# Kernel optimization log

Hardware: AMD Instinct MI355X
Metric: run time of the kernel (lower is better)

## Reference

```python
import jax, jax.numpy as jnp
import numpy as np
from jax import lax

K = 3
PAD = 1
DIL = 1
BN_EPS = 1e-5


def setup_inputs() -> dict:
    key = jax.random.key(0)
    ks = jax.random.split(key, 7)
    B, C, O, H, W = 4, 64, 64, 128, 128
    x = jax.random.normal(ks[0], (B, C, H, W), jnp.float32)
    # offset conv params (zero-init in the module; small random here to exercise bilinear sampling)
    w_off = jax.random.normal(ks[1], (2 * K * K, C, K, K), jnp.float32) * 0.01
    b_off = jax.random.normal(ks[2], (2 * K * K,), jnp.float32) * 0.01
    # deformable conv params
    w_dcn = jax.random.normal(ks[3], (O, C, K, K), jnp.float32) / np.sqrt(C * K * K).astype(np.float32)
    b_dcn = jax.random.normal(ks[4], (O,), jnp.float32) * 0.01
    # BatchNorm affine params
    gamma = 1.0 + 0.1 * jax.random.normal(ks[5], (O,), jnp.float32)
    beta = 0.1 * jax.random.normal(ks[6], (O,), jnp.float32)
    return dict(x=x, w_off=w_off, b_off=b_off, w_dcn=w_dcn, b_dcn=b_dcn, gamma=gamma, beta=beta)


def _conv2d(x, w):
    return lax.conv_general_dilated(
        x, w, window_strides=(1, 1), padding=[(PAD, PAD), (PAD, PAD)],
        rhs_dilation=(DIL, DIL), dimension_numbers=('NCHW', 'OIHW', 'NCHW'))


def _gather(x, iy, ix):
    # x: [B,C,H,W]; iy/ix: [B,K2,H,W] int32 (already clipped in-range)
    B, C, H, W = x.shape
    idx = (iy * W + ix).reshape(B, -1)          # [B, K2*H*W]
    xf = x.reshape(B, C, H * W)
    v = jax.vmap(lambda xb, ib: xb[:, ib])(xf, idx)  # [B, C, K2*H*W]
    return v.reshape(B, C, iy.shape[1], H, W)


def _deform_sample(x, offset):
    # torchvision DeformConv2d v1: offsets are (dy, dx) pairs per kernel tap, zero-padding bilinear.
    B, C, H, W = x.shape
    K2 = K * K
    off = offset.reshape(B, K2, 2, H, W)
    ky = jnp.repeat(jnp.arange(K), K)   # tap row index, k = ky*K + kx
    kx = jnp.tile(jnp.arange(K), K)
    py = off[:, :, 0] + (ky * DIL - PAD)[None, :, None, None] + jnp.arange(H)[None, None, :, None]
    px = off[:, :, 1] + (kx * DIL - PAD)[None, :, None, None] + jnp.arange(W)[None, None, None, :]
    y0 = jnp.floor(py)
    x0 = jnp.floor(px)
    wy = py - y0
    wx = px - x0
    y0i = y0.astype(jnp.int32)
    x0i = x0.astype(jnp.int32)
    acc = jnp.zeros((B, C, K2, H, W), x.dtype)
    for dy, dx in ((0, 0), (0, 1), (1, 0), (1, 1)):
        iy = y0i + dy
        ix = x0i + dx
        wgt = (wy if dy else 1.0 - wy) * (wx if dx else 1.0 - wx)
        valid = (iy >= 0) & (iy < H) & (ix >= 0) & (ix < W)
        v = _gather(x, jnp.clip(iy, 0, H - 1), jnp.clip(ix, 0, W - 1))
        acc = acc + v * (wgt * valid.astype(x.dtype))[:, None]
    return acc  # [B, C, K2, H, W]


def reference(x, w_off, b_off, w_dcn, b_dcn, gamma, beta):
    offset = _conv2d(x, w_off) + b_off[None, :, None, None]
    patches = _deform_sample(x, offset)                     # [B,C,K2,H,W]
    O = w_dcn.shape[0]
    out = jnp.einsum('bckhw,ock->bohw', patches, w_dcn.reshape(O, -1, K * K))
    out = out + b_dcn[None, :, None, None]
    # BatchNorm2d in training mode: biased batch statistics over (B,H,W)
    mean = out.mean(axis=(0, 2, 3), keepdims=True)
    var = out.var(axis=(0, 2, 3), keepdims=True)
    out = (out - mean) * lax.rsqrt(var + BN_EPS)
    out = out * gamma[None, :, None, None] + beta[None, :, None, None]
    return jax.nn.relu(out)
```

## Files before the change

kernel.cpp:

```cpp
#include <hip/hip_runtime.h>

#define HW   16384
#define WID  128
#define HEI  128
#define CIN  64
#define OCH  64

typedef __attribute__((ext_vector_type(8))) short bf16x8;
typedef __attribute__((ext_vector_type(4))) float f32x4;
typedef __attribute__((ext_vector_type(4))) int   i32x4;

__device__ __forceinline__ unsigned short f2bf(float f) {
    unsigned u = __float_as_uint(f);
    u += 0x7FFF + ((u >> 16) & 1);
    return (unsigned short)(u >> 16);
}
__device__ __forceinline__ float bf2f(short s) {
    return __uint_as_float(((unsigned)(unsigned short)s) << 16);
}

__global__ __launch_bounds__(256) void kprep(const float* __restrict__ x,
                                             const float* __restrict__ wdcn,
                                             const float* __restrict__ woff,
                                             unsigned short* __restrict__ xt,
                                             unsigned short* __restrict__ wpack,
                                             unsigned short* __restrict__ woffpack) {
    int blk = blockIdx.x;
    if (blk < 256) {
        int gp = blk * 256 + threadIdx.x;
        int b = gp >> 14;
        int hw = gp & (HW - 1);
        const float* xb = x + (size_t)b * CIN * HW + hw;
        unsigned short* o = xt + ((size_t)gp << 6);
#pragma unroll
        for (int c8 = 0; c8 < 8; c8++) {
            bf16x8 v;
#pragma unroll
            for (int j = 0; j < 8; j++)
                v[j] = (short)f2bf(xb[(size_t)(c8 * 8 + j) * HW]);
            *(bf16x8*)(o + c8 * 8) = v;
        }
    } else {
        int t = (blk - 256) * 256 + threadIdx.x;
        if (t < 36864) {
            int j  = t & 7;
            int l  = (t >> 3) & 63;
            int nt = (t >> 9) & 3;
            int s  = t >> 11;
            int k  = s * 32 + (l >> 4) * 8 + j;
            int o  = nt * 16 + (l & 15);
            int tap = k >> 6, c = k & 63;
            wpack[t] = f2bf(wdcn[o * 576 + c * 9 + tap]);
        } else {
            int u  = t - 36864;
            int j  = u & 7;
            int l  = (u >> 3) & 63;
            int nt = (u >> 9) & 1;
            int s  = u >> 10;
            int k  = s * 32 + (l >> 4) * 8 + j;
            int o  = nt * 16 + (l & 15);
            int tap = k >> 6, c = k & 63;
            float v = (o < 18) ? woff[o * 576 + c * 9 + tap] : 0.f;
            woffpack[u] = f2bf(v);
        }
    }
}

__global__ __launch_bounds__(256, 3) void kdcn(const unsigned short* __restrict__ xt,
                                               const unsigned short* __restrict__ wpack,
                                               const unsigned short* __restrict__ woffpack,
                                               const float* __restrict__ boff,
                                               const float* __restrict__ bdcn,
                                               float* __restrict__ conv,
                                               float* __restrict__ part) {
    __shared__ __align__(16) unsigned char smem[48384];

    int tid = threadIdx.x;
    int lane = tid & 63, wave = tid >> 6;
    int lr = lane & 15, hi = lane >> 4;

    int pixg = blockIdx.x * 32;
    int b = pixg >> 14;
    int hwb = pixg & (HW - 1);
    int h = hwb >> 7;
    int w0 = hwb & (WID - 1);

    {
        int g = lane >> 3, sub = lane & 7;
        int px = wave * 8 + g;
        int w = w0 + px;
        const unsigned char* xtb =
            (const unsigned char*)xt + (((size_t)b * HW) << 7) + sub * 16;
        unsigned char* prow = smem + px * 1152;
        unsigned swz = (unsigned)((px & 7) << 4);
#pragma unroll
        for (int tap = 0; tap < 9; tap++) {
            int sy = h + tap / 3 - 1;
            int sx = w + tap % 3 - 1;
            bool ok = ((unsigned)sy < HEI) && ((unsigned)sx < WID);
            bf16x8 v = {0, 0, 0, 0, 0, 0, 0, 0};
            if (ok) v = *(const bf16x8*)(xtb + ((sy * WID + sx) << 7));
            *(bf16x8*)(prow + ((unsigned)(tap * 128 + sub * 16) ^ swz)) = v;
        }
    }
    __syncthreads();

    {
        int mw = wave & 1, nw = wave >> 1;
        int oc = nw * 16 + lr;
        float ob = (oc < 18) ? boff[oc] : 0.f;
        f32x4 oacc = {ob, ob, ob, ob};
        unsigned swzr = (unsigned)((lr & 7) << 4);
        const unsigned short* wop = woffpack + (size_t)(nw * 64 + lane) * 8;
        int arow = (mw * 16 + lr) * 1152;
#pragma unroll
        for (int s = 0; s < 18; s++) {
            unsigned inblk = (unsigned)((s >> 1) * 128)
                           + (((unsigned)((s & 1) * 64 + hi * 16)) ^ swzr);
            bf16x8 a  = *(const bf16x8*)(smem + arow + inblk);
            bf16x8 wf = *(const bf16x8*)(wop + (size_t)s * 1024);
            oacc = __builtin_amdgcn_mfma_f32_16x16x32_bf16(a, wf, oacc, 0, 0, 0);
        }
        float* offLds = (float*)(smem + 46080);
        if (oc < 18) {
#pragma unroll
            for (int r = 0; r < 4; r++)
                offLds[(mw * 16 + hi * 4 + r) * 18 + oc] = oacc[r];
        }
    }
    __syncthreads();

    int* ti = (int*)(smem + 36864);
    {
        const float* offLds = (const float*)(smem + 46080);
        for (int item = tid; item < 288; item += 256) {
            int ppx = item / 9, tap = item - ppx * 9;
            float dy = offLds[ppx * 18 + tap * 2];
            float dx = offLds[ppx * 18 + tap * 2 + 1];
            float py  = dy + (float)(h + tap / 3 - 1);
            float pxf = dx + (float)(w0 + ppx + tap % 3 - 1);
            float y0f = floorf(py), x0f = floorf(pxf);
            float wy = py - y0f, wx = pxf - x0f;
            int y0 = (int)y0f, x0 = (int)x0f;
            float wy0 = ((unsigned)y0       < HEI) ? 1.f - wy : 0.f;
            float wy1 = ((unsigned)(y0 + 1) < HEI) ? wy       : 0.f;
            float wx0 = ((unsigned)x0       < WID) ? 1.f - wx : 0.f;
            float wx1 = ((unsigned)(x0 + 1) < WID) ? wx       : 0.f;
            int yc0 = min(max(y0, 0),     HEI - 1) * WID;
            int yc1 = min(max(y0 + 1, 0), HEI - 1) * WID;
            int xc0 = min(max(x0, 0),     WID - 1);
            int xc1 = min(max(x0 + 1, 0), WID - 1);
            int* t8 = ti + item * 8;
            t8[0] = (yc0 + xc0) << 7;
            t8[1] = (yc0 + xc1) << 7;
            t8[2] = (yc1 + xc0) << 7;
            t8[3] = (yc1 + xc1) << 7;
            float* f8 = (float*)t8;
            f8[4] = wy0 * wx0; f8[5] = wy0 * wx1;
            f8[6] = wy1 * wx0; f8[7] = wy1 * wx1;
        }
    }
    __syncthreads();

    bf16x8 bfrag[18];
    const unsigned short* wp = wpack + (size_t)(wave * 64 + lane) * 8;
#pragma unroll
    for (int s = 0; s < 18; s++)
        bfrag[s] = *(const bf16x8*)(wp + (size_t)s * 2048);
    float bias = bdcn[wave * 16 + lr];

    {
        int g = lane >> 3, sub = lane & 7;
        int px = wave * 8 + g;
        const unsigned char* xtb =
            (const unsigned char*)xt + (((size_t)b * HW) << 7) + sub * 16;
        unsigned char* prow = smem + px * 1152;
        unsigned swz = (unsigned)((px & 7) << 4);
        const int* tbase = ti + px * 72;
#pragma unroll
        for (int tap = 0; tap < 9; tap++) {
            i32x4 t4 = *(const i32x4*)(tbase + tap * 8);
            f32x4 w4 = *(const f32x4*)(tbase + tap * 8 + 4);
            bf16x8 c00 = *(const bf16x8*)(xtb + t4[0]);
            bf16x8 c01 = *(const bf16x8*)(xtb + t4[1]);
            bf16x8 c10 = *(const bf16x8*)(xtb + t4[2]);
            bf16x8 c11 = *(const bf16x8*)(xtb + t4[3]);
            bf16x8 v;
#pragma unroll
            for (int j = 0; j < 8; j++) {
                float sv = w4[0] * bf2f(c00[j]) + w4[1] * bf2f(c01[j])
                         + w4[2] * bf2f(c10[j]) + w4[3] * bf2f(c11[j]);
                v[j] = (short)f2bf(sv);
            }
            *(bf16x8*)(prow + ((unsigned)(tap * 128 + sub * 16) ^ swz)) = v;
        }
    }
    __syncthreads();

    f32x4 acc0 = {bias, bias, bias, bias};
    f32x4 acc1 = acc0;
    unsigned swzr = (unsigned)((lr & 7) << 4);
#pragma unroll
    for (int s = 0; s < 18; s++) {
        unsigned inblk = (unsigned)((s >> 1) * 128)
                       + (((unsigned)((s & 1) * 64 + hi * 16)) ^ swzr);
        bf16x8 a0 = *(const bf16x8*)(smem + lr * 1152 + inblk);
        bf16x8 a1 = *(const bf16x8*)(smem + (16 + lr) * 1152 + inblk);
        acc0 = __builtin_amdgcn_mfma_f32_16x16x32_bf16(a0, bfrag[s], acc0, 0, 0, 0);
        acc1 = __builtin_amdgcn_mfma_f32_16x16x32_bf16(a1, bfrag[s], acc1, 0, 0, 0);
    }
    __syncthreads();

    float* ldsC = (float*)smem;
    {
        int o = wave * 16 + lr;
        int pxb = hi * 4;
#pragma unroll
        for (int r = 0; r < 4; r++) {
            ldsC[o * 33 + pxb + r]      = acc0[r];
            ldsC[o * 33 + 16 + pxb + r] = acc1[r];
        }
    }
    __syncthreads();
    {
        int px4 = (tid & 7) * 4;
#pragma unroll
        for (int pass = 0; pass < 2; pass++) {
            int oo = (tid >> 3) + pass * 32;
            float4 v;
            v.x = ldsC[oo * 33 + px4];
            v.y = ldsC[oo * 33 + px4 + 1];
            v.z = ldsC[oo * 33 + px4 + 2];
            v.w = ldsC[oo * 33 + px4 + 3];
            *(float4*)(conv + ((size_t)b * OCH + oo) * HW + hwb + px4) = v;
        }
    }

    {
        float s  = acc0[0] + acc0[1] + acc0[2] + acc0[3]
                 + acc1[0] + acc1[1] + acc1[2] + acc1[3];
        float s2 = acc0[0]*acc0[0] + acc0[1]*acc0[1] + acc0[2]*acc0[2] + acc0[3]*acc0[3]
                 + acc1[0]*acc1[0] + acc1[1]*acc1[1] + acc1[2]*acc1[2] + acc1[3]*acc1[3];
        s  += __shfl_xor(s, 16);  s2 += __shfl_xor(s2, 16);
        s  += __shfl_xor(s, 32);  s2 += __shfl_xor(s2, 32);
        if (hi == 0) {
            int c = wave * 16 + lr;
            part[(size_t)c * 2048 + blockIdx.x]        = s;
            part[(size_t)(64 + c) * 2048 + blockIdx.x] = s2;
        }
    }
}

__global__ __launch_bounds__(256) void kred(const float* __restrict__ part,
                                            float* __restrict__ stats) {
    int row = blockIdx.x;
    int tid = threadIdx.x;
    const float* p = part + (size_t)row * 2048;
    float s = 0.f;
#pragma unroll
    for (int i = 0; i < 8; i++) s += p[tid + i * 256];
#pragma unroll
    for (int d = 1; d < 64; d <<= 1) s += __shfl_xor(s, d);
    __shared__ float red[4];
    if ((tid & 63) == 0) red[tid >> 6] = s;
    __syncthreads();
    if (tid == 0) stats[row] = red[0] + red[1] + red[2] + red[3];
}

__global__ __launch_bounds__(256) void kapply(float* __restrict__ conv,
                                              const float* __restrict__ stats,
                                              const float* __restrict__ gamma,
                                              const float* __restrict__ beta) {
    int t = blockIdx.x * 256 + threadIdx.x;
    int c = (t >> 12) & 63;
    float mean = stats[c] * (1.f / 65536.f);
    float var  = stats[64 + c] * (1.f / 65536.f) - mean * mean;
    float rstd = rsqrtf(var + 1e-5f);
    float sc = rstd * gamma[c];
    float sh = beta[c] - mean * sc;
    float4 v = ((float4*)conv)[t];
    float4 r;
    r.x = fmaxf(v.x * sc + sh, 0.f);
    r.y = fmaxf(v.y * sc + sh, 0.f);
    r.z = fmaxf(v.z * sc + sh, 0.f);
    r.w = fmaxf(v.w * sc + sh, 0.f);
    ((float4*)conv)[t] = r;
}

extern "C" void kernel_launch(void* const* d_in, const int* in_sizes, int n_in,
                              void* d_out, int out_size, void* d_ws, size_t ws_size,
                              hipStream_t stream) {
    const float* x     = (const float*)d_in[0];
    const float* woff  = (const float*)d_in[1];
    const float* boff  = (const float*)d_in[2];
    const float* wdcn  = (const float*)d_in[3];
    const float* bdcn  = (const float*)d_in[4];
    const float* gamma = (const float*)d_in[5];
    const float* beta  = (const float*)d_in[6];
    float* out = (float*)d_out;

    unsigned char* ws = (unsigned char*)d_ws;
    unsigned short* xt       = (unsigned short*)ws;
    unsigned short* wpack    = (unsigned short*)(ws + 8388608);
    unsigned short* woffpack = (unsigned short*)(ws + 8462336);
    float*          part     = (float*)(ws + 8499200);
    float*          stats    = (float*)(ws + 9547776);

    hipLaunchKernelGGL(kprep,  dim3(472),  dim3(256), 0, stream,
                       x, wdcn, woff, xt, wpack, woffpack);
    hipLaunchKernelGGL(kdcn,   dim3(2048), dim3(256), 0, stream,
                       xt, wpack, woffpack, boff, bdcn, out, part);
    hipLaunchKernelGGL(kred,   dim3(128),  dim3(256), 0, stream, part, stats);
    hipLaunchKernelGGL(kapply, dim3(4096), dim3(256), 0, stream,
                       out, stats, gamma, beta);
}
```

Baseline: 56.52 us.

## Compute bilinear sampling coefficients per lane and drop LDS tap table

Removes the shared-memory table of per-tap gather indices and bilinear weights. Each of the 8 lanes that handle one pixel now recomputes the coordinates and weights from the offset LDS values. This drops one barrier and shrinks LDS from about 48 KB to 39 KB, so the launch bound is raised to 4 blocks per CU. It also hoists the weight-fragment loads ahead of the barrier. The cost is redundant ALU work per lane and higher register pressure, which could cause spills under the tighter occupancy bound.

After: 56.88 us. Within noise of the previous version (+0.6%).

```diff
diff --git a/kernel.cpp b/kernel.cpp
--- a/kernel.cpp
+++ b/kernel.cpp
@@ -66,14 +66,14 @@
     }
 }
 
-__global__ __launch_bounds__(256, 3) void kdcn(const unsigned short* __restrict__ xt,
+__global__ __launch_bounds__(256, 4) void kdcn(const unsigned short* __restrict__ xt,
                                                const unsigned short* __restrict__ wpack,
                                                const unsigned short* __restrict__ woffpack,
                                                const float* __restrict__ boff,
                                                const float* __restrict__ bdcn,
                                                float* __restrict__ conv,
                                                float* __restrict__ part) {
-    __shared__ __align__(16) unsigned char smem[48384];
+    __shared__ __align__(16) unsigned char smem[39168];
 
     int tid = threadIdx.x;
     int lane = tid & 63, wave = tid >> 6;
@@ -121,24 +121,37 @@
             bf16x8 wf = *(const bf16x8*)(wop + (size_t)s * 1024);
             oacc = __builtin_amdgcn_mfma_f32_16x16x32_bf16(a, wf, oacc, 0, 0, 0);
         }
-        float* offLds = (float*)(smem + 46080);
+        float* offLds = (float*)(smem + 36864);
         if (oc < 18) {
 #pragma unroll
             for (int r = 0; r < 4; r++)
                 offLds[(mw * 16 + hi * 4 + r) * 18 + oc] = oacc[r];
         }
     }
-    __syncthreads();
-
-    int* ti = (int*)(smem + 36864);
-    {
-        const float* offLds = (const float*)(smem + 46080);
-        for (int item = tid; item < 288; item += 256) {
-            int ppx = item / 9, tap = item - ppx * 9;
-            float dy = offLds[ppx * 18 + tap * 2];
-            float dx = offLds[ppx * 18 + tap * 2 + 1];
+
+    bf16x8 bfrag[18];
+    const unsigned short* wp = wpack + (size_t)(wave * 64 + lane) * 8;
+#pragma unroll
+    for (int s = 0; s < 18; s++)
+        bfrag[s] = *(const bf16x8*)(wp + (size_t)s * 2048);
+    float bias = bdcn[wave * 16 + lr];
+    __syncthreads();
+
+    {
+        int g = lane >> 3, sub = lane & 7;
+        int px = wave * 8 + g;
+        int w = w0 + px;
+        const unsigned char* xtb =
+            (const unsigned char*)xt + (((size_t)b * HW) << 7) + sub * 16;
+        unsigned char* prow = smem + px * 1152;
+        unsigned swz = (unsigned)((px & 7) << 4);
+        const float* offL = (const float*)(smem + 36864) + px * 18;
+#pragma unroll
+        for (int tap = 0; tap < 9; tap++) {
+            float dy = offL[tap * 2];
+            float dx = offL[tap * 2 + 1];
             float py  = dy + (float)(h + tap / 3 - 1);
-            float pxf = dx + (float)(w0 + ppx + tap % 3 - 1);
+            float pxf = dx + (float)(w + tap % 3 - 1);
             float y0f = floorf(py), x0f = floorf(pxf);
             float wy = py - y0f, wx = pxf - x0f;
             int y0 = (int)y0f, x0 = (int)x0f;
@@ -150,46 +163,17 @@
             int yc1 = min(max(y0 + 1, 0), HEI - 1) * WID;
             int xc0 = min(max(x0, 0),     WID - 1);
             int xc1 = min(max(x0 + 1, 0), WID - 1);
-            int* t8 = ti + item * 8;
-            t8[0] = (yc0 + xc0) << 7;
-            t8[1] = (yc0 + xc1) << 7;
-            t8[2] = (yc1 + xc0) << 7;
-            t8[3] = (yc1 + xc1) << 7;
-            float* f8 = (float*)t8;
-            f8[4] = wy0 * wx0; f8[5] = wy0 * wx1;
-            f8[6] = wy1 * wx0; f8[7] = wy1 * wx1;
-        }
-    }
-    __syncthreads();
-
-    bf16x8 bfrag[18];
-    const unsigned short* wp = wpack + (size_t)(wave * 64 + lane) * 8;
-#pragma unroll
-    for (int s = 0; s < 18; s++)
-        bfrag[s] = *(const bf16x8*)(wp + (size_t)s * 2048);
-    float bias = bdcn[wave * 16 + lr];
-
-    {
-        int g = lane >> 3, sub = lane & 7;
-        int px = wave * 8 + g;
-        const unsigned char* xtb =
-            (const unsigned char*)xt + (((size_t)b * HW) << 7) + sub * 16;
-        unsigned char* prow = smem + px * 1152;
-        unsigned swz = (unsigned)((px & 7) << 4);
-        const int* tbase = ti + px * 72;
-#pragma unroll
-        for (int tap = 0; tap < 9; tap++) {
-            i32x4 t4 = *(const i32x4*)(tbase + tap * 8);
-            f32x4 w4 = *(const f32x4*)(tbase + tap * 8 + 4);
-            bf16x8 c00 = *(const bf16x8*)(xtb + t4[0]);
-            bf16x8 c01 = *(const bf16x8*)(xtb + t4[1]);
-            bf16x8 c10 = *(const bf16x8*)(xtb + t4[2]);
-            bf16x8 c11 = *(const bf16x8*)(xtb + t4[3]);
+            float w00 = wy0 * wx0, w01 = wy0 * wx1;
+            float w10 = wy1 * wx0, w11 = wy1 * wx1;
+            bf16x8 c00 = *(const bf16x8*)(xtb + ((yc0 + xc0) << 7));
+            bf16x8 c01 = *(const bf16x8*)(xtb + ((yc0 + xc1) << 7));
+            bf16x8 c10 = *(const bf16x8*)(xtb + ((yc1 + xc0) << 7));
+            bf16x8 c11 = *(const bf16x8*)(xtb + ((yc1 + xc1) << 7));
             bf16x8 v;
 #pragma unroll
             for (int j = 0; j < 8; j++) {
-                float sv = w4[0] * bf2f(c00[j]) + w4[1] * bf2f(c01[j])
-                         + w4[2] * bf2f(c10[j]) + w4[3] * bf2f(c11[j]);
+                float sv = w00 * bf2f(c00[j]) + w01 * bf2f(c01[j])
+                         + w10 * bf2f(c10[j]) + w11 * bf2f(c11[j]);
                 v[j] = (short)f2bf(sv);
             }
             *(bf16x8*)(prow + ((unsigned)(tap * 128 + sub * 16) ^ swz)) = v;
```
